# Kernel tuning notes

Hardware: AMD Instinct MI355X
Metric: run time of the kernel (lower is better)

The kernel has to match this reference:

```python
import jax, jax.numpy as jnp
import numpy as np

DEPTH, HEADS, DIM_HEAD = 3, 8, 64
DIM = 512
MAX_SEQ = 2048
INNER = HEADS * DIM_HEAD  # 512
FF_HID = 4 * DIM          # 2048
EPS = 1e-5


def sparsemax(z):
    # z: (..., n); sparsemax projection onto the simplex (Martins & Astudillo 2016)
    n = z.shape[-1]
    z_sorted = jnp.flip(jnp.sort(z, axis=-1), axis=-1)            # descending
    cs = jnp.cumsum(z_sorted, axis=-1)
    ks = jnp.arange(1, n + 1, dtype=z.dtype)
    support = 1.0 + ks * z_sorted > cs                            # bool
    k_z = jnp.sum(support, axis=-1, keepdims=True)                # int support size
    cs_k = jnp.take_along_axis(cs, k_z - 1, axis=-1)
    tau = (cs_k - 1.0) / k_z.astype(z.dtype)
    return jnp.maximum(z - tau, 0.0)


def layernorm(x, g, b):
    mu = jnp.mean(x, axis=-1, keepdims=True)
    var = jnp.mean(jnp.square(x - mu), axis=-1, keepdims=True)
    return (x - mu) * jax.lax.rsqrt(var + EPS) * g + b


def setup_inputs() -> dict:
    key = jax.random.key(0)
    ks = jax.random.split(key, 12)
    s = 0.02
    inp = {
        "x": jax.random.normal(ks[0], (8, 1024, DIM), dtype=jnp.float32),
        "proj_w": jax.random.normal(ks[1], (DIM, DIM), dtype=jnp.float32) * s,
        "proj_b": jnp.zeros((DIM,), dtype=jnp.float32),
        "pos_emb": jax.random.normal(ks[2], (MAX_SEQ, DIM), dtype=jnp.float32) * s,
        "ln1_g": jnp.ones((DEPTH, DIM), dtype=jnp.float32),
        "ln1_b": jnp.zeros((DEPTH, DIM), dtype=jnp.float32),
        "wqkv": jax.random.normal(ks[3], (DEPTH, DIM, 3 * INNER), dtype=jnp.float32) * s,
        "wout": jax.random.normal(ks[4], (DEPTH, INNER, DIM), dtype=jnp.float32) * s,
        "bout": jnp.zeros((DEPTH, DIM), dtype=jnp.float32),
        "ln2_g": jnp.ones((DEPTH, DIM), dtype=jnp.float32),
        "ln2_b": jnp.zeros((DEPTH, DIM), dtype=jnp.float32),
        "w1": jax.random.normal(ks[5], (DEPTH, DIM, 2 * FF_HID), dtype=jnp.float32) * s,
        "b1": jnp.zeros((DEPTH, 2 * FF_HID), dtype=jnp.float32),
        "w2": jax.random.normal(ks[6], (DEPTH, FF_HID, DIM), dtype=jnp.float32) * s,
        "b2": jnp.zeros((DEPTH, DIM), dtype=jnp.float32),
    }
    return inp


def reference(x, proj_w, proj_b, pos_emb, ln1_g, ln1_b, wqkv, wout, bout,
              ln2_g, ln2_b, w1, b1, w2, b2):
    B, S, D = x.shape
    scale = DIM_HEAD ** -0.5
    x = x @ proj_w + proj_b                       # projection
    x = x + pos_emb[:S][None, :, :]               # positional embedding
    for l in range(DEPTH):
        # --- attention block (Residual(PreNorm(Attention))) ---
        h = layernorm(x, ln1_g[l], ln1_b[l])
        qkv = h @ wqkv[l]                         # (B,S,3*INNER)
        q, k, v = jnp.split(qkv, 3, axis=-1)
        rs = lambda t: t.reshape(B, S, HEADS, DIM_HEAD).transpose(0, 2, 1, 3)
        q, k, v = rs(q), rs(k), rs(v)             # (B,H,S,Dh)
        sim = jnp.einsum('bhid,bhjd->bhij', q, k) * scale
        attn = sparsemax(sim)
        out = jnp.einsum('bhij,bhjd->bhid', attn, v)
        out = out.transpose(0, 2, 1, 3).reshape(B, S, INNER)
        x = x + (out @ wout[l] + bout[l])
        # --- feedforward block (Residual(PreNorm(GEGLU FFN))) ---
        h = layernorm(x, ln2_g[l], ln2_b[l])
        hh = h @ w1[l] + b1[l]                    # (B,S,2*FF_HID)
        a, g = jnp.split(hh, 2, axis=-1)
        ff = (a * jax.nn.gelu(g, approximate=False)) @ w2[l] + b2[l]
        x = x + ff
    return jnp.mean(x, axis=1)                    # (B, D) mean pool
```

## Files before the change

### kernel.cpp

```cpp
#include <hip/hip_runtime.h>
#include <stdint.h>

typedef unsigned short u16;
typedef __attribute__((ext_vector_type(8))) short short8;
typedef __attribute__((ext_vector_type(4))) float f32x4;

__device__ __forceinline__ float bf2f(u16 u){
  union { unsigned u; float f; } v; v.u = ((unsigned)u) << 16; return v.f;
}
__device__ __forceinline__ u16 f2bf(float f){
  union { float f; unsigned u; } v; v.f = f;
  unsigned u = v.u;
  return (u16)((u + 0x7FFFu + ((u >> 16) & 1u)) >> 16);
}
__device__ __forceinline__ void g2lds16(const u16* g, u16* lds){
  __builtin_amdgcn_global_load_lds(
      (const __attribute__((address_space(1))) unsigned int*)g,
      (__attribute__((address_space(3))) unsigned int*)lds, 16, 0, 0);
}

__global__ void k_flag(const unsigned* __restrict__ ln1g, int* __restrict__ flag){
  if (threadIdx.x == 0 && blockIdx.x == 0)
    *flag = (ln1g[0] == 0x3F800000u) ? 0 : 1;
}

__global__ void k_cvt_f32(const void* __restrict__ src, float* __restrict__ dst, int n,
                          const int* __restrict__ flag){
  int i = blockIdx.x * blockDim.x + threadIdx.x;
  if (i < n) dst[i] = (*flag) ? bf2f(((const u16*)src)[i]) : ((const float*)src)[i];
}
__global__ void k_cvt_bf16(const void* __restrict__ src, u16* __restrict__ dst, int n,
                           const int* __restrict__ flag){
  int i = blockIdx.x * blockDim.x + threadIdx.x;
  if (i < n) dst[i] = (*flag) ? ((const u16*)src)[i] : f2bf(((const float*)src)[i]);
}

__global__ void k_transpose(const void* __restrict__ src, u16* __restrict__ dst,
                            int K, int N, const int* __restrict__ flag){
  __shared__ u16 tile[32][33];
  int n0 = blockIdx.x * 32, k0 = blockIdx.y * 32;
  size_t zsrc = (size_t)blockIdx.z * K * N;
  size_t zdst = (size_t)blockIdx.z * N * K;
  int tx = threadIdx.x & 31, ty = threadIdx.x >> 5;
  bool isbf = (*flag) != 0;
  const float* sf = (const float*)src; const u16* sb = (const u16*)src;
  #pragma unroll
  for (int p = 0; p < 4; ++p){
    int kk = k0 + p*8 + ty, nn = n0 + tx;
    size_t idx = zsrc + (size_t)kk * N + nn;
    tile[tx][p*8+ty] = isbf ? sb[idx] : f2bf(sf[idx]);
  }
  __syncthreads();
  #pragma unroll
  for (int p = 0; p < 4; ++p){
    int nn = n0 + p*8 + ty, kk = k0 + tx;
    dst[zdst + (size_t)nn * K + kk] = tile[p*8+ty][tx];
  }
}

__global__ void k_vt(const u16* __restrict__ src, u16* __restrict__ dst){
  __shared__ u16 tile[32][33];
  int d0 = blockIdx.x * 32, s0 = blockIdx.y * 32;
  size_t base = (size_t)blockIdx.z * 65536;
  int tx = threadIdx.x & 31, ty = threadIdx.x >> 5;
  #pragma unroll
  for (int p = 0; p < 4; ++p)
    tile[tx][p*8+ty] = src[base + (size_t)(s0 + p*8 + ty) * 64 + d0 + tx];
  __syncthreads();
  #pragma unroll
  for (int p = 0; p < 4; ++p)
    dst[base + (size_t)(d0 + p*8 + ty) * 1024 + s0 + tx] = tile[p*8+ty][tx];
}

__global__ __launch_bounds__(256) void k_ln(const float* __restrict__ x,
                                            const float* __restrict__ g,
                                            const float* __restrict__ b,
                                            u16* __restrict__ out){
  int row = blockIdx.x, tid = threadIdx.x;
  const float* xr = x + (size_t)row * 512;
  float x0 = xr[tid], x1 = xr[tid + 256];
  float s = x0 + x1, ss = x0*x0 + x1*x1;
  #pragma unroll
  for (int off = 1; off < 64; off <<= 1){ s += __shfl_xor(s, off, 64); ss += __shfl_xor(ss, off, 64); }
  __shared__ float as_[4], bs_[4];
  int wv = tid >> 6, lane = tid & 63;
  if (lane == 0){ as_[wv] = s; bs_[wv] = ss; }
  __syncthreads();
  s = as_[0] + as_[1] + as_[2] + as_[3];
  ss = bs_[0] + bs_[1] + bs_[2] + bs_[3];
  float mu = s * (1.f/512.f);
  float var = ss * (1.f/512.f) - mu*mu;
  float rs = rsqrtf(var + 1e-5f);
  out[(size_t)row*512 + tid]       = f2bf((x0 - mu) * rs * g[tid]       + b[tid]);
  out[(size_t)row*512 + tid + 256] = f2bf((x1 - mu) * rs * g[tid + 256] + b[tid + 256]);
}

__global__ __launch_bounds__(256) void k_gemm(const u16* __restrict__ A,
                                              const u16* __restrict__ Wt, int K, int mode,
                                              float* __restrict__ xres, u16* __restrict__ out16,
                                              const float* __restrict__ bias,
                                              const float* __restrict__ pos){
  __shared__ u16 As[128*64];
  __shared__ u16 Bs[128*64];
  const int tid = threadIdx.x;
  const int wv = tid >> 6, lane = tid & 63;
  const int lm = lane & 15, lq = lane >> 4;
  const int wm = (wv >> 1) * 64, wn = (wv & 1) * 64;
  const int m0 = blockIdx.y * 128, n0 = blockIdx.x * 128;
  const int lrow = lane >> 3;
  const int scol = ((lane & 7) ^ lrow) << 3;
  f32x4 acc[4][4];
  #pragma unroll
  for (int i = 0; i < 4; ++i)
    #pragma unroll
    for (int j = 0; j < 4; ++j){ f32x4 z = {0.f,0.f,0.f,0.f}; acc[i][j] = z; }

  for (int k0 = 0; k0 < K; k0 += 64){
    #pragma unroll
    for (int it = 0; it < 4; ++it){
      int ci = wv*4 + it;
      int row = ci*8 + lrow;
      g2lds16(&A [(size_t)(m0 + row) * K + k0 + scol], &As[ci*512]);
      g2lds16(&Wt[(size_t)(n0 + row) * K + k0 + scol], &Bs[ci*512]);
    }
    __syncthreads();
    #pragma unroll
    for (int kk = 0; kk < 2; ++kk){
      short8 af[4], bf[4];
      #pragma unroll
      for (int t = 0; t < 4; ++t){
        int cs = ((kk*4 + lq) ^ (lm & 7)) << 3;
        af[t] = *(const short8*)&As[(wm + t*16 + lm)*64 + cs];
        bf[t] = *(const short8*)&Bs[(wn + t*16 + lm)*64 + cs];
      }
      #pragma unroll
      for (int i = 0; i < 4; ++i)
        #pragma unroll
        for (int j = 0; j < 4; ++j)
          acc[i][j] = __builtin_amdgcn_mfma_f32_16x16x32_bf16(af[i], bf[j], acc[i][j], 0, 0, 0);
    }
    __syncthreads();
  }
  #pragma unroll
  for (int i = 0; i < 4; ++i)
    #pragma unroll
    for (int j = 0; j < 4; ++j)
      #pragma unroll
      for (int r = 0; r < 4; ++r){
        int row = m0 + wm + i*16 + lq*4 + r;
        int col = n0 + wn + j*16 + lm;
        float v = acc[i][j][r];
        if (mode == 0){
          xres[(size_t)row*512 + col] = v + bias[col] + pos[(size_t)(row & 1023)*512 + col];
        } else if (mode == 1){
          int part = col >> 9, within = col & 511;
          int head = within >> 6, dh = within & 63;
          int b = row >> 10, s = row & 1023;
          out16[(size_t)part*4194304 + (((size_t)(b*8 + head)*1024 + s) << 6) + dh] = f2bf(v);
        } else {
          size_t idx = (size_t)row*512 + col;
          xres[idx] = xres[idx] + v + bias[col];
        }
      }
}

__global__ __launch_bounds__(256) void k_gemm64(const u16* __restrict__ A,
                                                const u16* __restrict__ Wt, int K, int mode,
                                                float* __restrict__ xres,
                                                const float* __restrict__ bias,
                                                const float* __restrict__ pos){
  __shared__ u16 As[64*64];
  __shared__ u16 Bs[128*64];
  const int tid = threadIdx.x;
  const int wv = tid >> 6, lane = tid & 63;
  const int lm = lane & 15, lq = lane >> 4;
  const int wm = (wv >> 1) * 32, wn = (wv & 1) * 64;
  const int m0 = blockIdx.y * 64, n0 = blockIdx.x * 128;
  const int lrow = lane >> 3;
  const int scol = ((lane & 7) ^ lrow) << 3;
  f32x4 acc[2][4];
  #pragma unroll
  for (int i = 0; i < 2; ++i)
    #pragma unroll
    for (int j = 0; j < 4; ++j){ f32x4 z = {0.f,0.f,0.f,0.f}; acc[i][j] = z; }

  for (int k0 = 0; k0 < K; k0 += 64){
    #pragma unroll
    for (int it = 0; it < 2; ++it){
      int ci = wv*2 + it;
      int row = ci*8 + lrow;
      g2lds16(&A[(size_t)(m0 + row) * K + k0 + scol], &As[ci*512]);
    }
    #pragma unroll
    for (int it = 0; it < 4; ++it){
      int ci = wv*4 + it;
      int row = ci*8 + lrow;
      g2lds16(&Wt[(size_t)(n0 + row) * K + k0 + scol], &Bs[ci*512]);
    }
    __syncthreads();
    #pragma unroll
    for (int kk = 0; kk < 2; ++kk){
      short8 af[2], bf[4];
      int cs = ((kk*4 + lq) ^ (lm & 7)) << 3;
      #pragma unroll
      for (int t = 0; t < 2; ++t)
        af[t] = *(const short8*)&As[(wm + t*16 + lm)*64 + cs];
      #pragma unroll
      for (int t = 0; t < 4; ++t)
        bf[t] = *(const short8*)&Bs[(wn + t*16 + lm)*64 + cs];
      #pragma unroll
      for (int i = 0; i < 2; ++i)
        #pragma unroll
        for (int j = 0; j < 4; ++j)
          acc[i][j] = __builtin_amdgcn_mfma_f32_16x16x32_bf16(af[i], bf[j], acc[i][j], 0, 0, 0);
    }
    __syncthreads();
  }
  #pragma unroll
  for (int i = 0; i < 2; ++i)
    #pragma unroll
    for (int j = 0; j < 4; ++j)
      #pragma unroll
      for (int r = 0; r < 4; ++r){
        int row = m0 + wm + i*16 + lq*4 + r;
        int col = n0 + wn + j*16 + lm;
        float v = acc[i][j][r];
        if (mode == 0){
          xres[(size_t)row*512 + col] = v + bias[col] + pos[(size_t)(row & 1023)*512 + col];
        } else {
          size_t idx = (size_t)row*512 + col;
          xres[idx] = xres[idx] + v + bias[col];
        }
      }
}

__global__ __launch_bounds__(256) void k_ff1_geglu(const u16* __restrict__ A,
                                                   const u16* __restrict__ W1t,
                                                   const float* __restrict__ b1,
                                                   u16* __restrict__ ffh){
  __shared__ u16 As[128*64];
  __shared__ u16 Ba[128*64];
  __shared__ u16 Bg[128*64];
  const int tid = threadIdx.x;
  const int wv = tid >> 6, lane = tid & 63;
  const int lm = lane & 15, lq = lane >> 4;
  const int wm = (wv >> 1) * 64, wn = (wv & 1) * 64;
  const int m0 = blockIdx.y * 128, n0 = blockIdx.x * 128;
  const int lrow = lane >> 3;
  const int scol = ((lane & 7) ^ lrow) << 3;
  const int K = 512;
  f32x4 aa[4][4], ag[4][4];
  #pragma unroll
  for (int i = 0; i < 4; ++i)
    #pragma unroll
    for (int j = 0; j < 4; ++j){ f32x4 z = {0.f,0.f,0.f,0.f}; aa[i][j] = z; ag[i][j] = z; }
  for (int k0 = 0; k0 < K; k0 += 64){
    #pragma unroll
    for (int it = 0; it < 4; ++it){
      int ci = wv*4 + it;
      int row = ci*8 + lrow;
      g2lds16(&A  [(size_t)(m0 + row) * K + k0 + scol], &As[ci*512]);
      g2lds16(&W1t[(size_t)(n0 + row) * K + k0 + scol], &Ba[ci*512]);
      g2lds16(&W1t[(size_t)(2048 + n0 + row) * K + k0 + scol], &Bg[ci*512]);
    }
    __syncthreads();
    #pragma unroll
    for (int kk = 0; kk < 2; ++kk){
      short8 af[4], ba[4], bg[4];
      #pragma unroll
      for (int t = 0; t < 4; ++t){
        int cs = ((kk*4 + lq) ^ (lm & 7)) << 3;
        af[t] = *(const short8*)&As[(wm + t*16 + lm)*64 + cs];
        ba[t] = *(const short8*)&Ba[(wn + t*16 + lm)*64 + cs];
        bg[t] = *(const short8*)&Bg[(wn + t*16 + lm)*64 + cs];
      }
      #pragma unroll
      for (int i = 0; i < 4; ++i)
        #pragma unroll
        for (int j = 0; j < 4; ++j){
          aa[i][j] = __builtin_amdgcn_mfma_f32_16x16x32_bf16(af[i], ba[j], aa[i][j], 0, 0, 0);
          ag[i][j] = __builtin_amdgcn_mfma_f32_16x16x32_bf16(af[i], bg[j], ag[i][j], 0, 0, 0);
        }
    }
    __syncthreads();
  }
  #pragma unroll
  for (int i = 0; i < 4; ++i)
    #pragma unroll
    for (int j = 0; j < 4; ++j)
      #pragma unroll
      for (int r = 0; r < 4; ++r){
        int row = m0 + wm + i*16 + lq*4 + r;
        int n = n0 + wn + j*16 + lm;
        float a = aa[i][j][r] + b1[n];
        float g = ag[i][j][r] + b1[2048 + n];
        float ge = 0.5f * g * (1.0f + erff(g * 0.70710678118654752440f));
        ffh[(size_t)row*2048 + n] = f2bf(a * ge);
      }
}

__global__ __launch_bounds__(256) void k_qk(const u16* __restrict__ qb,
                                            const u16* __restrict__ kb,
                                            u16* __restrict__ S, int bh0){
  __shared__ u16 As[128*64];
  __shared__ u16 Bs[128*64];
  const int tid = threadIdx.x;
  const int wv = tid >> 6, lane = tid & 63;
  const int lm = lane & 15, lq = lane >> 4;
  const int wm = (wv >> 1) * 64, wn = (wv & 1) * 64;
  const int m0 = blockIdx.y * 128, n0 = blockIdx.x * 128;
  const int lrow = lane >> 3;
  const int scol = ((lane & 7) ^ lrow) << 3;
  const size_t base = (size_t)(bh0 + blockIdx.z) * 65536;
  f32x4 acc[4][4];
  #pragma unroll
  for (int i = 0; i < 4; ++i)
    #pragma unroll
    for (int j = 0; j < 4; ++j){ f32x4 z = {0.f,0.f,0.f,0.f}; acc[i][j] = z; }

  #pragma unroll
  for (int it = 0; it < 4; ++it){
    int ci = wv*4 + it;
    int row = ci*8 + lrow;
    g2lds16(&qb[base + (size_t)(m0 + row) * 64 + scol], &As[ci*512]);
    g2lds16(&kb[base + (size_t)(n0 + row) * 64 + scol], &Bs[ci*512]);
  }
  __syncthreads();
  #pragma unroll
  for (int kk = 0; kk < 2; ++kk){
    short8 af[4], bf[4];
    #pragma unroll
    for (int t = 0; t < 4; ++t){
      int cs = ((kk*4 + lq) ^ (lm & 7)) << 3;
      af[t] = *(const short8*)&As[(wm + t*16 + lm)*64 + cs];
      bf[t] = *(const short8*)&Bs[(wn + t*16 + lm)*64 + cs];
    }
    #pragma unroll
    for (int i = 0; i < 4; ++i)
      #pragma unroll
      for (int j = 0; j < 4; ++j)
        acc[i][j] = __builtin_amdgcn_mfma_f32_16x16x32_bf16(af[i], bf[j], acc[i][j], 0, 0, 0);
  }
  size_t sb = (size_t)blockIdx.z * 1048576;
  #pragma unroll
  for (int i = 0; i < 4; ++i)
    #pragma unroll
    for (int j = 0; j < 4; ++j)
      #pragma unroll
      for (int r = 0; r < 4; ++r){
        int row = m0 + wm + i*16 + lq*4 + r;
        int col = n0 + wn + j*16 + lm;
        S[sb + (size_t)row*1024 + col] = f2bf(acc[i][j][r] * 0.125f);
      }
}

__global__ __launch_bounds__(256) void k_spmax(const u16* __restrict__ S,
                                               u16* __restrict__ P){
  const int lane = threadIdx.x & 63;
  const int row = blockIdx.x * 4 + (threadIdx.x >> 6);
  const u16* src = S + (size_t)row * 1024 + lane * 16;
  u16 zb[16];
  *(uint4*)zb       = *(const uint4*)src;
  *(uint4*)(zb + 8) = *(const uint4*)(src + 8);
  float z[16];
  #pragma unroll
  for (int i = 0; i < 16; ++i) z[i] = bf2f(zb[i]);
  bool act[16];
  #pragma unroll
  for (int i = 0; i < 16; ++i) act[i] = true;
  float prevc = -1.f, tau = 0.f;
  for (int it = 0; it < 64; ++it){
    float s = 0.f, c = 0.f;
    #pragma unroll
    for (int i = 0; i < 16; ++i) if (act[i]){ s += z[i]; c += 1.f; }
    #pragma unroll
    for (int off = 1; off < 64; off <<= 1){ s += __shfl_xor(s, off, 64); c += __shfl_xor(c, off, 64); }
    tau = (s - 1.0f) / c;
    if (c == prevc) break;
    prevc = c;
    #pragma unroll
    for (int i = 0; i < 16; ++i) act[i] = z[i] > tau;
  }
  u16 tmp[16];
  #pragma unroll
  for (int i = 0; i < 16; ++i){
    float p = z[i] - tau; p = p > 0.f ? p : 0.f;
    tmp[i] = f2bf(p);
  }
  u16* dst = P + (size_t)row * 1024 + lane * 16;
  *(uint4*)dst       = *(const uint4*)tmp;
  *(uint4*)(dst + 8) = *(const uint4*)(tmp + 8);
}

__global__ __launch_bounds__(256) void k_pv(const u16* __restrict__ P,
                                            const u16* __restrict__ vt,
                                            u16* __restrict__ aout, int bh0){
  __shared__ u16 As[64*64];
  __shared__ u16 Bs[64*64];
  const int tid = threadIdx.x;
  const int wv = tid >> 6, lane = tid & 63;
  const int lm = lane & 15, lq = lane >> 4;
  const int m0 = blockIdx.x * 64;
  const int bh = bh0 + blockIdx.y;
  const size_t pbase = (size_t)blockIdx.y * 1048576;
  const size_t vbase = (size_t)bh * 65536;
  const int lrow = lane >> 3;
  const int scol = ((lane & 7) ^ lrow) << 3;
  f32x4 acc[4];
  #pragma unroll
  for (int j = 0; j < 4; ++j){ f32x4 z = {0.f,0.f,0.f,0.f}; acc[j] = z; }

  for (int k0 = 0; k0 < 1024; k0 += 64){
    #pragma unroll
    for (int it = 0; it < 2; ++it){
      int ci = wv*2 + it;
      int row = ci*8 + lrow;
      g2lds16(&P [pbase + (size_t)(m0 + row) * 1024 + k0 + scol], &As[ci*512]);
      g2lds16(&vt[vbase + (size_t)row * 1024 + k0 + scol],        &Bs[ci*512]);
    }
    __syncthreads();
    #pragma unroll
    for (int kk = 0; kk < 2; ++kk){
      int csa = ((kk*4 + lq) ^ (lm & 7)) << 3;
      short8 af = *(const short8*)&As[(wv*16 + lm)*64 + csa];
      #pragma unroll
      for (int j = 0; j < 4; ++j){
        short8 bf = *(const short8*)&Bs[(j*16 + lm)*64 + csa];
        acc[j] = __builtin_amdgcn_mfma_f32_16x16x32_bf16(af, bf, acc[j], 0, 0, 0);
      }
    }
    __syncthreads();
  }
  int b = bh >> 3, h = bh & 7;
  #pragma unroll
  for (int j = 0; j < 4; ++j)
    #pragma unroll
    for (int r = 0; r < 4; ++r){
      int s = m0 + wv*16 + lq*4 + r;
      int d = j*16 + lm;
      aout[((size_t)(b*1024 + s))*512 + h*64 + d] = f2bf(acc[j][r]);
    }
}

__global__ __launch_bounds__(256) void k_attn(const u16* __restrict__ qb,
                                              const u16* __restrict__ kb,
                                              const u16* __restrict__ vb,
                                              u16* __restrict__ aout){
  extern __shared__ char smem[];
  float* sc = (float*)smem;
  u16*  P   = (u16*)smem;
  u16*  Qs  = (u16*)(smem + 131072);
  u16*  KVs = (u16*)(smem + 131072 + 4608);
  const int tid = threadIdx.x;
  const int wv = tid >> 6, lane = tid & 63;
  const int lm = lane & 15, lq = lane >> 4;
  const int bh = blockIdx.y, s0 = blockIdx.x * 32;
  const size_t base = (size_t)bh * 65536;
  {
    int r = tid >> 3, c = tid & 7;
    *(uint4*)&Qs[r*72 + (c << 3)] = *(const uint4*)&qb[base + (size_t)(s0 + r)*64 + (c << 3)];
  }
  for (int kt = 0; kt < 16; ++kt){
    __syncthreads();
    #pragma unroll
    for (int it = 0; it < 2; ++it){
      int s = it*256 + tid; int r = s >> 3, c = s & 7;
      *(uint4*)&KVs[r*72 + (c << 3)] =
          *(const uint4*)&kb[base + (size_t)(kt*64 + r)*64 + (c << 3)];
    }
    __syncthreads();
    f32x4 accs[2];
    { f32x4 z = {0.f,0.f,0.f,0.f}; accs[0] = z; accs[1] = z; }
    #pragma unroll
    for (int kk = 0; kk < 2; ++kk){
      short8 bfk = *(const short8*)&KVs[(wv*16 + lm)*72 + kk*32 + lq*8];
      #pragma unroll
      for (int mt = 0; mt < 2; ++mt){
        short8 af = *(const short8*)&Qs[(mt*16 + lm)*72 + kk*32 + lq*8];
        accs[mt] = __builtin_amdgcn_mfma_f32_16x16x32_bf16(af, bfk, accs[mt], 0, 0, 0);
      }
    }
    #pragma unroll
    for (int mt = 0; mt < 2; ++mt)
      #pragma unroll
      for (int r = 0; r < 4; ++r){
        int row = mt*16 + lq*4 + r;
        int col = kt*64 + wv*16 + lm;
        sc[row*1024 + (((col >> 2) ^ (row & 7)) << 2) + (col & 3)] = accs[mt][r] * 0.125f;
      }
  }
  __syncthreads();
  for (int rr = 0; rr < 8; ++rr){
    int row = wv*8 + rr;
    float z[16];
    #pragma unroll
    for (int i = 0; i < 16; ++i){
      int col = lane + (i << 6);
      z[i] = sc[row*1024 + (((col >> 2) ^ (row & 7)) << 2) + (col & 3)];
    }
    bool act[16];
    #pragma unroll
    for (int i = 0; i < 16; ++i) act[i] = true;
    float prevc = -1.f, tau = 0.f;
    for (int it = 0; it < 64; ++it){
      float s = 0.f, c = 0.f;
      #pragma unroll
      for (int i = 0; i < 16; ++i) if (act[i]){ s += z[i]; c += 1.f; }
      #pragma unroll
      for (int off = 1; off < 64; off <<= 1){ s += __shfl_xor(s, off, 64); c += __shfl_xor(c, off, 64); }
      tau = (s - 1.0f) / c;
      if (c == prevc) break;
      prevc = c;
      #pragma unroll
      for (int i = 0; i < 16; ++i) act[i] = z[i] > tau;
    }
    #pragma unroll
    for (int i = 0; i < 16; ++i){
      int col = lane + (i << 6);
      float p = z[i] - tau; p = p > 0.f ? p : 0.f;
      P[row*2048 + (((col >> 3) ^ (row & 7)) << 3) + (col & 7)] = f2bf(p);
    }
  }
  f32x4 acco[2];
  { f32x4 z = {0.f,0.f,0.f,0.f}; acco[0] = z; acco[1] = z; }
  for (int kt = 0; kt < 16; ++kt){
    __syncthreads();
    {
      int dc = tid >> 6, key = tid & 63;
      const u16* src = &vb[base + (size_t)(kt*64 + key)*64 + dc*16];
      u16 tmp[16];
      *(uint4*)tmp       = *(const uint4*)src;
      *(uint4*)(tmp + 8) = *(const uint4*)(src + 8);
      #pragma unroll
      for (int j = 0; j < 16; ++j) KVs[(dc*16 + j)*72 + key] = tmp[j];
    }
    __syncthreads();
    #pragma unroll
    for (int kk = 0; kk < 2; ++kk){
      short8 bfv = *(const short8*)&KVs[(wv*16 + lm)*72 + kk*32 + lq*8];
      #pragma unroll
      for (int mt = 0; mt < 2; ++mt){
        int m = mt*16 + lm;
        int k = kt*64 + kk*32 + lq*8;
        short8 af = *(const short8*)&P[m*2048 + (((k >> 3) ^ (m & 7)) << 3)];
        acco[mt] = __builtin_amdgcn_mfma_f32_16x16x32_bf16(af, bfv, acco[mt], 0, 0, 0);
      }
    }
  }
  int b = bh >> 3, h = bh & 7;
  #pragma unroll
  for (int mt = 0; mt < 2; ++mt)
    #pragma unroll
    for (int r = 0; r < 4; ++r){
      int row = mt*16 + lq*4 + r;
      int s = s0 + row;
      aout[((size_t)(b*1024 + s))*512 + h*64 + wv*16 + lm] = f2bf(acco[mt][r]);
    }
}

__global__ __launch_bounds__(256) void k_pool1(const float* __restrict__ xres,
                                               float* __restrict__ part){
  int b = blockIdx.y, ch = blockIdx.x, tid = threadIdx.x;
  float a0 = 0.f, a1 = 0.f;
  for (int i = 0; i < 64; ++i){
    const float* r = xres + ((size_t)(b*1024 + ch*64 + i)) * 512;
    a0 += r[tid]; a1 += r[tid + 256];
  }
  part[((size_t)(b*16 + ch))*512 + tid]       = a0;
  part[((size_t)(b*16 + ch))*512 + tid + 256] = a1;
}
__global__ __launch_bounds__(512) void k_pool2(const float* __restrict__ part,
                                               void* __restrict__ out,
                                               const int* __restrict__ flag){
  int b = blockIdx.x, d = threadIdx.x;
  float s = 0.f;
  for (int c = 0; c < 16; ++c) s += part[((size_t)(b*16 + c))*512 + d];
  s *= (1.0f/1024.0f);
  if (*flag) ((u16*)out)[b*512 + d] = f2bf(s);
  else       ((float*)out)[b*512 + d] = s;
}

extern "C" void kernel_launch(void* const* d_in, const int* in_sizes, int n_in,
                              void* d_out, int out_size, void* d_ws, size_t ws_size,
                              hipStream_t stream){
  (void)in_sizes; (void)n_in; (void)out_size;
  char* w = (char*)d_ws;
  size_t off = 0;
  auto alloc = [&](size_t bytes) -> char* {
    char* p = w + off;
    off += (bytes + 255) & ~(size_t)255;
    return p;
  };
  int*   flag  = (int*)  alloc(4);
  float* xres  = (float*)alloc((size_t)8192*512*4);
  u16*   hb    = (u16*)  alloc((size_t)8192*512*2);
  u16*   qb    = (u16*)  alloc((size_t)8388608);
  u16*   kb    = (u16*)  alloc((size_t)8388608);
  u16*   vb    = (u16*)  alloc((size_t)8388608);
  u16*   aoutb = (u16*)  alloc((size_t)8388608);
  u16*   ffh   = qb;
  u16*   pwT   = (u16*)  alloc((size_t)512*512*2);
  u16*   wqkvT = (u16*)  alloc((size_t)3*1536*512*2);
  u16*   woutT = (u16*)  alloc((size_t)3*512*512*2);
  u16*   w1T   = (u16*)  alloc((size_t)3*4096*512*2);
  u16*   w2T   = (u16*)  alloc((size_t)3*512*2048*2);
  float* posf  = (float*)alloc((size_t)1024*512*4);
  float* pbf   = (float*)alloc(512*4);
  float* ln1gf = (float*)alloc(1536*4);
  float* ln1bf = (float*)alloc(1536*4);
  float* ln2gf = (float*)alloc(1536*4);
  float* ln2bf = (float*)alloc(1536*4);
  float* boutf = (float*)alloc(1536*4);
  float* b1f   = (float*)alloc(12288*4);
  float* b2f   = (float*)alloc(1536*4);
  float* part  = (float*)alloc((size_t)8*16*512*4);
  u16*   vt    = (u16*)  alloc((size_t)8388608);

  int chunk = 0;
  u16* Sbuf = nullptr; u16* Pbuf = nullptr;
  {
    size_t rem = (ws_size > off) ? (ws_size - off) : 0;
    for (int c = 64; c >= 8; c >>= 1){
      size_t need = (size_t)c * 1048576 * 4 + 512;
      if (need <= rem){
        Sbuf = (u16*)alloc((size_t)c * 1048576 * 2);
        Pbuf = (u16*)alloc((size_t)c * 1048576 * 2);
        chunk = c;
        break;
      }
    }
  }

  const void* x_raw = d_in[0];  const void* projw = d_in[1];  const void* projb = d_in[2];
  const void* pose  = d_in[3];  const void* ln1g  = d_in[4];  const void* ln1b  = d_in[5];
  const void* wqkv  = d_in[6];  const void* wout  = d_in[7];  const void* bout  = d_in[8];
  const void* ln2g  = d_in[9];  const void* ln2b  = d_in[10]; const void* w1    = d_in[11];
  const void* b1    = d_in[12]; const void* w2    = d_in[13]; const void* b2    = d_in[14];

  k_flag<<<1, 1, 0, stream>>>((const unsigned*)ln1g, flag);

  k_transpose<<<dim3(16, 16, 1), 256, 0, stream>>>(projw, pwT,   512,  512, flag);
  k_transpose<<<dim3(48, 16, 3), 256, 0, stream>>>(wqkv,  wqkvT, 512, 1536, flag);
  k_transpose<<<dim3(16, 16, 3), 256, 0, stream>>>(wout,  woutT, 512,  512, flag);
  k_transpose<<<dim3(128,16, 3), 256, 0, stream>>>(w1,    w1T,   512, 4096, flag);
  k_transpose<<<dim3(16, 64, 3), 256, 0, stream>>>(w2,    w2T,  2048,  512, flag);

  k_cvt_f32<<<2,    256, 0, stream>>>(projb, pbf,    512,    flag);
  k_cvt_f32<<<2048, 256, 0, stream>>>(pose,  posf,   524288, flag);
  k_cvt_f32<<<6,    256, 0, stream>>>(ln1g,  ln1gf,  1536,   flag);
  k_cvt_f32<<<6,    256, 0, stream>>>(ln1b,  ln1bf,  1536,   flag);
  k_cvt_f32<<<6,    256, 0, stream>>>(ln2g,  ln2gf,  1536,   flag);
  k_cvt_f32<<<6,    256, 0, stream>>>(ln2b,  ln2bf,  1536,   flag);
  k_cvt_f32<<<6,    256, 0, stream>>>(bout,  boutf,  1536,   flag);
  k_cvt_f32<<<48,   256, 0, stream>>>(b1,    b1f,    12288,  flag);
  k_cvt_f32<<<6,    256, 0, stream>>>(b2,    b2f,    1536,   flag);
  k_cvt_bf16<<<16384, 256, 0, stream>>>(x_raw, hb, 4194304, flag);

  k_gemm64<<<dim3(4, 128), 256, 0, stream>>>(hb, pwT, 512, 0, xres, pbf, posf);

  for (int l = 0; l < 3; ++l){
    k_ln<<<8192, 256, 0, stream>>>(xres, ln1gf + l*512, ln1bf + l*512, hb);
    k_gemm<<<dim3(12, 64), 256, 0, stream>>>(hb, wqkvT + (size_t)l*1536*512, 512, 1,
                                             nullptr, qb, nullptr, nullptr);
    if (chunk){
      k_vt<<<dim3(2, 32, 64), 256, 0, stream>>>(vb, vt);
      for (int bh0 = 0; bh0 < 64; bh0 += chunk){
        k_qk<<<dim3(8, 8, chunk), 256, 0, stream>>>(qb, kb, Sbuf, bh0);
        k_spmax<<<chunk*256, 256, 0, stream>>>(Sbuf, Pbuf);
        k_pv<<<dim3(16, chunk), 256, 0, stream>>>(Pbuf, vt, aoutb, bh0);
      }
    } else {
      k_attn<<<dim3(32, 64), 256, 144896, stream>>>(qb, kb, vb, aoutb);
    }
    k_gemm64<<<dim3(4, 128), 256, 0, stream>>>(aoutb, woutT + (size_t)l*512*512, 512, 2,
                                               xres, boutf + l*512, nullptr);
    k_ln<<<8192, 256, 0, stream>>>(xres, ln2gf + l*512, ln2bf + l*512, hb);
    k_ff1_geglu<<<dim3(16, 64), 256, 0, stream>>>(hb, w1T + (size_t)l*4096*512,
                                                  b1f + l*4096, ffh);
    k_gemm64<<<dim3(4, 128), 256, 0, stream>>>(ffh, w2T + (size_t)l*512*2048, 2048, 2,
                                               xres, b2f + l*512, nullptr);
  }
  k_pool1<<<dim3(16, 8), 256, 0, stream>>>(xres, part);
  k_pool2<<<8, 512, 0, stream>>>(part, d_out, flag);
}
```

Before: 1.244 ms.

## Fuse QK^T with sparsemax in registers and shrink GEGLU FF1 M-tile

Replaces the separate QK^T score kernel and row-wise sparsemax kernel with one kernel. It keeps a 32x1024 score strip in registers, with each wave owning 256 columns, and finds tau by iterative thresholding using a cross-wave LDS reduction. This removes the bf16 score buffer write and read and one launch per chunk, though each iteration now needs block-wide syncs and register pressure rises. It also halves the M tile of the GEGLU FF1 GEMM to 64 rows, doubling the grid for better occupancy and CU coverage. The cost is more re-reads of the weight tiles.

```diff
diff --git a/kernel.cpp b/kernel.cpp
--- a/kernel.cpp
+++ b/kernel.cpp
@@ -234,48 +234,55 @@
       }
 }
 
-__global__ __launch_bounds__(256) void k_ff1_geglu(const u16* __restrict__ A,
-                                                   const u16* __restrict__ W1t,
-                                                   const float* __restrict__ b1,
-                                                   u16* __restrict__ ffh){
-  __shared__ u16 As[128*64];
+__global__ __launch_bounds__(256) void k_ff1_geglu64(const u16* __restrict__ A,
+                                                     const u16* __restrict__ W1t,
+                                                     const float* __restrict__ b1,
+                                                     u16* __restrict__ ffh){
+  __shared__ u16 As[64*64];
   __shared__ u16 Ba[128*64];
   __shared__ u16 Bg[128*64];
   const int tid = threadIdx.x;
   const int wv = tid >> 6, lane = tid & 63;
   const int lm = lane & 15, lq = lane >> 4;
-  const int wm = (wv >> 1) * 64, wn = (wv & 1) * 64;
-  const int m0 = blockIdx.y * 128, n0 = blockIdx.x * 128;
+  const int wm = (wv >> 1) * 32, wn = (wv & 1) * 64;
+  const int m0 = blockIdx.y * 64, n0 = blockIdx.x * 128;
   const int lrow = lane >> 3;
   const int scol = ((lane & 7) ^ lrow) << 3;
   const int K = 512;
-  f32x4 aa[4][4], ag[4][4];
-  #pragma unroll
-  for (int i = 0; i < 4; ++i)
+  f32x4 aa[2][4], ag[2][4];
+  #pragma unroll
+  for (int i = 0; i < 2; ++i)
     #pragma unroll
     for (int j = 0; j < 4; ++j){ f32x4 z = {0.f,0.f,0.f,0.f}; aa[i][j] = z; ag[i][j] = z; }
   for (int k0 = 0; k0 < K; k0 += 64){
+    #pragma unroll
+    for (int it = 0; it < 2; ++it){
+      int ci = wv*2 + it;
+      int row = ci*8 + lrow;
+      g2lds16(&A[(size_t)(m0 + row) * K + k0 + scol], &As[ci*512]);
+    }
     #pragma unroll
     for (int it = 0; it < 4; ++it){
       int ci = wv*4 + it;
       int row = ci*8 + lrow;
-      g2lds16(&A  [(size_t)(m0 + row) * K + k0 + scol], &As[ci*512]);
-      g2lds16(&W1t[(size_t)(n0 + row) * K + k0 + scol], &Ba[ci*512]);
+      g2lds16(&W1t[(size_t)(n0 + row) * K + k0 + scol],        &Ba[ci*512]);
       g2lds16(&W1t[(size_t)(2048 + n0 + row) * K + k0 + scol], &Bg[ci*512]);
     }
     __syncthreads();
     #pragma unroll
     for (int kk = 0; kk < 2; ++kk){
-      short8 af[4], ba[4], bg[4];
+      short8 af[2], ba[4], bg[4];
+      int cs = ((kk*4 + lq) ^ (lm & 7)) << 3;
+      #pragma unroll
+      for (int t = 0; t < 2; ++t)
+        af[t] = *(const short8*)&As[(wm + t*16 + lm)*64 + cs];
       #pragma unroll
       for (int t = 0; t < 4; ++t){
-        int cs = ((kk*4 + lq) ^ (lm & 7)) << 3;
-        af[t] = *(const short8*)&As[(wm + t*16 + lm)*64 + cs];
         ba[t] = *(const short8*)&Ba[(wn + t*16 + lm)*64 + cs];
         bg[t] = *(const short8*)&Bg[(wn + t*16 + lm)*64 + cs];
       }
       #pragma unroll
-      for (int i = 0; i < 4; ++i)
+      for (int i = 0; i < 2; ++i)
         #pragma unroll
         for (int j = 0; j < 4; ++j){
           aa[i][j] = __builtin_amdgcn_mfma_f32_16x16x32_bf16(af[i], ba[j], aa[i][j], 0, 0, 0);
@@ -285,7 +292,7 @@
     __syncthreads();
   }
   #pragma unroll
-  for (int i = 0; i < 4; ++i)
+  for (int i = 0; i < 2; ++i)
     #pragma unroll
     for (int j = 0; j < 4; ++j)
       #pragma unroll
@@ -299,97 +306,132 @@
       }
 }
 
-__global__ __launch_bounds__(256) void k_qk(const u16* __restrict__ qb,
-                                            const u16* __restrict__ kb,
-                                            u16* __restrict__ S, int bh0){
-  __shared__ u16 As[128*64];
-  __shared__ u16 Bs[128*64];
+__global__ __launch_bounds__(256) void k_qkspmax(const u16* __restrict__ qb,
+                                                 const u16* __restrict__ kb,
+                                                 u16* __restrict__ P, int bh0){
+  __shared__ u16 Qs[4][32*64];
+  __shared__ u16 Ks[4][64*64];
+  __shared__ float red_s[4][32];
+  __shared__ float red_c[4][32];
+  __shared__ float tauL[32];
+  __shared__ int flagL;
   const int tid = threadIdx.x;
   const int wv = tid >> 6, lane = tid & 63;
   const int lm = lane & 15, lq = lane >> 4;
-  const int wm = (wv >> 1) * 64, wn = (wv & 1) * 64;
-  const int m0 = blockIdx.y * 128, n0 = blockIdx.x * 128;
-  const int lrow = lane >> 3;
-  const int scol = ((lane & 7) ^ lrow) << 3;
-  const size_t base = (size_t)(bh0 + blockIdx.z) * 65536;
-  f32x4 acc[4][4];
-  #pragma unroll
-  for (int i = 0; i < 4; ++i)
-    #pragma unroll
-    for (int j = 0; j < 4; ++j){ f32x4 z = {0.f,0.f,0.f,0.f}; acc[i][j] = z; }
+  const int lrow = lane >> 3, c8 = lane & 7;
+  const int m0 = blockIdx.x * 32;
+  const size_t base = (size_t)(bh0 + blockIdx.y) * 65536;
+  const size_t pb = (size_t)blockIdx.y * 1048576;
 
   #pragma unroll
   for (int it = 0; it < 4; ++it){
-    int ci = wv*4 + it;
-    int row = ci*8 + lrow;
-    g2lds16(&qb[base + (size_t)(m0 + row) * 64 + scol], &As[ci*512]);
-    g2lds16(&kb[base + (size_t)(n0 + row) * 64 + scol], &Bs[ci*512]);
-  }
-  __syncthreads();
-  #pragma unroll
-  for (int kk = 0; kk < 2; ++kk){
-    short8 af[4], bf[4];
-    #pragma unroll
-    for (int t = 0; t < 4; ++t){
+    int row = it*8 + lrow;
+    g2lds16(&qb[base + (size_t)(m0 + row) * 64 + ((c8 ^ (row & 7)) << 3)], &Qs[wv][it*512]);
+  }
+  f32x4 acc[4][2][4];
+  #pragma unroll
+  for (int kt = 0; kt < 4; ++kt)
+    #pragma unroll
+    for (int i = 0; i < 2; ++i)
+      #pragma unroll
+      for (int j = 0; j < 4; ++j){ f32x4 z = {0.f,0.f,0.f,0.f}; acc[kt][i][j] = z; }
+
+  for (int kt = 0; kt < 4; ++kt){
+    if (kt) __builtin_amdgcn_s_waitcnt(0);
+    int kbase = (wv*4 + kt) * 64;
+    #pragma unroll
+    for (int it = 0; it < 8; ++it){
+      int row = it*8 + lrow;
+      g2lds16(&kb[base + (size_t)(kbase + row) * 64 + ((c8 ^ (row & 7)) << 3)], &Ks[wv][it*512]);
+    }
+    __builtin_amdgcn_s_waitcnt(0);
+    #pragma unroll
+    for (int kk = 0; kk < 2; ++kk){
       int cs = ((kk*4 + lq) ^ (lm & 7)) << 3;
-      af[t] = *(const short8*)&As[(wm + t*16 + lm)*64 + cs];
-      bf[t] = *(const short8*)&Bs[(wn + t*16 + lm)*64 + cs];
-    }
-    #pragma unroll
-    for (int i = 0; i < 4; ++i)
+      short8 af[2], bf[4];
+      #pragma unroll
+      for (int t = 0; t < 2; ++t) af[t] = *(const short8*)&Qs[wv][(t*16 + lm)*64 + cs];
+      #pragma unroll
+      for (int t = 0; t < 4; ++t) bf[t] = *(const short8*)&Ks[wv][(t*16 + lm)*64 + cs];
+      #pragma unroll
+      for (int i = 0; i < 2; ++i)
+        #pragma unroll
+        for (int j = 0; j < 4; ++j)
+          acc[kt][i][j] = __builtin_amdgcn_mfma_f32_16x16x32_bf16(af[i], bf[j], acc[kt][i][j], 0, 0, 0);
+    }
+  }
+  #pragma unroll
+  for (int kt = 0; kt < 4; ++kt)
+    #pragma unroll
+    for (int i = 0; i < 2; ++i)
       #pragma unroll
       for (int j = 0; j < 4; ++j)
-        acc[i][j] = __builtin_amdgcn_mfma_f32_16x16x32_bf16(af[i], bf[j], acc[i][j], 0, 0, 0);
-  }
-  size_t sb = (size_t)blockIdx.z * 1048576;
-  #pragma unroll
-  for (int i = 0; i < 4; ++i)
-    #pragma unroll
-    for (int j = 0; j < 4; ++j)
+        #pragma unroll
+        for (int r = 0; r < 4; ++r)
+          acc[kt][i][j][r] *= 0.125f;
+
+  float tauRow[8];
+  #pragma unroll
+  for (int i = 0; i < 8; ++i) tauRow[i] = -3.0e38f;
+  float myPrevC = -1.f;
+  for (int iter = 0; iter < 64; ++iter){
+    #pragma unroll
+    for (int mt = 0; mt < 2; ++mt)
       #pragma unroll
       for (int r = 0; r < 4; ++r){
-        int row = m0 + wm + i*16 + lq*4 + r;
-        int col = n0 + wn + j*16 + lm;
-        S[sb + (size_t)row*1024 + col] = f2bf(acc[i][j][r] * 0.125f);
-      }
-}
-
-__global__ __launch_bounds__(256) void k_spmax(const u16* __restrict__ S,
-                                               u16* __restrict__ P){
-  const int lane = threadIdx.x & 63;
-  const int row = blockIdx.x * 4 + (threadIdx.x >> 6);
-  const u16* src = S + (size_t)row * 1024 + lane * 16;
-  u16 zb[16];
-  *(uint4*)zb       = *(const uint4*)src;
-  *(uint4*)(zb + 8) = *(const uint4*)(src + 8);
-  float z[16];
-  #pragma unroll
-  for (int i = 0; i < 16; ++i) z[i] = bf2f(zb[i]);
-  bool act[16];
-  #pragma unroll
-  for (int i = 0; i < 16; ++i) act[i] = true;
-  float prevc = -1.f, tau = 0.f;
-  for (int it = 0; it < 64; ++it){
-    float s = 0.f, c = 0.f;
-    #pragma unroll
-    for (int i = 0; i < 16; ++i) if (act[i]){ s += z[i]; c += 1.f; }
-    #pragma unroll
-    for (int off = 1; off < 64; off <<= 1){ s += __shfl_xor(s, off, 64); c += __shfl_xor(c, off, 64); }
-    tau = (s - 1.0f) / c;
-    if (c == prevc) break;
-    prevc = c;
-    #pragma unroll
-    for (int i = 0; i < 16; ++i) act[i] = z[i] > tau;
-  }
-  u16 tmp[16];
-  #pragma unroll
-  for (int i = 0; i < 16; ++i){
-    float p = z[i] - tau; p = p > 0.f ? p : 0.f;
-    tmp[i] = f2bf(p);
-  }
-  u16* dst = P + (size_t)row * 1024 + lane * 16;
-  *(uint4*)dst       = *(const uint4*)tmp;
-  *(uint4*)(dst + 8) = *(const uint4*)(tmp + 8);
+        float t = tauRow[mt*4 + r];
+        float s = 0.f, c = 0.f;
+        #pragma unroll
+        for (int kt = 0; kt < 4; ++kt)
+          #pragma unroll
+          for (int j = 0; j < 4; ++j){
+            float zv = acc[kt][mt][j][r];
+            if (zv > t){ s += zv; c += 1.f; }
+          }
+        #pragma unroll
+        for (int off = 1; off < 16; off <<= 1){
+          s += __shfl_xor(s, off, 64); c += __shfl_xor(c, off, 64);
+        }
+        if (lm == 0){
+          int row = mt*16 + lq*4 + r;
+          red_s[wv][row] = s; red_c[wv][row] = c;
+        }
+      }
+    __syncthreads();
+    if (wv == 0){
+      bool conv = true;
+      if (lane < 32){
+        float S = red_s[0][lane] + red_s[1][lane] + red_s[2][lane] + red_s[3][lane];
+        float C = red_c[0][lane] + red_c[1][lane] + red_c[2][lane] + red_c[3][lane];
+        tauL[lane] = (S - 1.0f) / C;
+        conv = (C == myPrevC);
+        myPrevC = C;
+      }
+      unsigned long long msk = __ballot(conv);
+      if (lane == 0) flagL = (msk == ~0ull) ? 1 : 0;
+    }
+    __syncthreads();
+    #pragma unroll
+    for (int mt = 0; mt < 2; ++mt)
+      #pragma unroll
+      for (int r = 0; r < 4; ++r)
+        tauRow[mt*4 + r] = tauL[mt*16 + lq*4 + r];
+    if (flagL) break;
+  }
+  #pragma unroll
+  for (int kt = 0; kt < 4; ++kt)
+    #pragma unroll
+    for (int mt = 0; mt < 2; ++mt)
+      #pragma unroll
+      for (int j = 0; j < 4; ++j)
+        #pragma unroll
+        for (int r = 0; r < 4; ++r){
+          float p = acc[kt][mt][j][r] - tauRow[mt*4 + r];
+          p = p > 0.f ? p : 0.f;
+          int row = m0 + mt*16 + lq*4 + r;
+          int col = wv*256 + kt*64 + j*16 + lm;
+          P[pb + (size_t)row*1024 + col] = f2bf(p);
+        }
 }
 
 __global__ __launch_bounds__(256) void k_pv(const u16* __restrict__ P,
@@ -617,13 +659,12 @@
   u16*   vt    = (u16*)  alloc((size_t)8388608);
 
   int chunk = 0;
-  u16* Sbuf = nullptr; u16* Pbuf = nullptr;
+  u16* Pbuf = nullptr;
   {
     size_t rem = (ws_size > off) ? (ws_size - off) : 0;
     for (int c = 64; c >= 8; c >>= 1){
-      size_t need = (size_t)c * 1048576 * 4 + 512;
+      size_t need = (size_t)c * 1048576 * 2 + 512;
       if (need <= rem){
-        Sbuf = (u16*)alloc((size_t)c * 1048576 * 2);
         Pbuf = (u16*)alloc((size_t)c * 1048576 * 2);
         chunk = c;
         break;
@@ -665,8 +706,7 @@
     if (chunk){
       k_vt<<<dim3(2, 32, 64), 256, 0, stream>>>(vb, vt);
       for (int bh0 = 0; bh0 < 64; bh0 += chunk){
-        k_qk<<<dim3(8, 8, chunk), 256, 0, stream>>>(qb, kb, Sbuf, bh0);
-        k_spmax<<<chunk*256, 256, 0, stream>>>(Sbuf, Pbuf);
+        k_qkspmax<<<dim3(32, chunk), 256, 0, stream>>>(qb, kb, Pbuf, bh0);
         k_pv<<<dim3(16, chunk), 256, 0, stream>>>(Pbuf, vt, aoutb, bh0);
       }
     } else {
@@ -675,8 +715,8 @@
     k_gemm64<<<dim3(4, 128), 256, 0, stream>>>(aoutb, woutT + (size_t)l*512*512, 512, 2,
                                                xres, boutf + l*512, nullptr);
     k_ln<<<8192, 256, 0, stream>>>(xres, ln2gf + l*512, ln2bf + l*512, hb);
-    k_ff1_geglu<<<dim3(16, 64), 256, 0, stream>>>(hb, w1T + (size_t)l*4096*512,
-                                                  b1f + l*4096, ffh);
+    k_ff1_geglu64<<<dim3(16, 128), 256, 0, stream>>>(hb, w1T + (size_t)l*4096*512,
+                                                     b1f + l*4096, ffh);
     k_gemm64<<<dim3(4, 128), 256, 0, stream>>>(ffh, w2T + (size_t)l*512*2048, 2048, 2,
                                                xres, b2f + l*512, nullptr);
   }
```

New measurement: 1.237 ms. About the same (-0.6%).
